# Optimization experiments

Measured on AMD Instinct MI355X. Metric: run time of the kernel, lower is better.

The kernel has to match this reference:

```python
import jax, jax.numpy as jnp
import numpy as np

N_NODES = 50000
N_EDGES = 1_600_000
N_DIMS = 64
INTERACT = ((0,), (1,), (0, 1))  # interact index tuples over [hidden_vi, hidden_vj]


def setup_inputs() -> dict:
    key = jax.random.key(0)
    k1, k2, k3 = jax.random.split(key, 3)
    hidden = jax.random.normal(k1, (1, N_NODES, N_DIMS), dtype=jnp.float32)
    pos_weight = jax.random.uniform(k2, (len(INTERACT), N_DIMS), dtype=jnp.float32)
    neg_weight = jax.random.uniform(k3, (len(INTERACT), N_DIMS), dtype=jnp.float32)
    rng = np.random.default_rng(0)
    vi = np.sort(rng.integers(0, N_NODES, size=N_EDGES)).astype(np.int32)  # sorted by vi
    vj = rng.integers(0, N_NODES, size=N_EDGES).astype(np.int32)
    rel = rng.integers(0, 500, size=N_EDGES).astype(np.int32)
    idx = np.zeros(N_EDGES, dtype=np.int32)  # batch_size == 1
    # (idx, vi, vj, rel, idx_vi, idx_vj, new_idx_e2vi, new_idx_e2vj)
    selected_edges = np.stack([idx, vi, vj, rel, vi, vj, vi, vj], axis=1)
    return {
        "hidden": hidden,
        "pos_weight": pos_weight,
        "neg_weight": neg_weight,
        "selected_edges": jnp.asarray(selected_edges),
    }


def _scorer(inputs, pos_weight, neg_weight):
    # inputs: list of [E, D]; returns per-edge scalar logits [E]
    pos_xs, neg_xs = [], []
    for idxs in INTERACT:
        pos_x = jnp.ones((), jnp.float32)
        neg_x = jnp.ones((), jnp.float32)
        for i in idxs:
            pos_x = pos_x * jnp.maximum(inputs[i], 0)
            neg_x = neg_x * (-jnp.minimum(inputs[i], 0))
        pos_xs.append(pos_x)
        neg_xs.append(neg_x)
    pos_xs = jnp.stack(pos_xs, axis=-2)  # [E, n_prod, D]
    neg_xs = jnp.stack(neg_xs, axis=-2)
    logits = jnp.sum(pos_xs * pos_weight, axis=(-2, -1)) - jnp.sum(neg_xs * neg_weight, axis=(-2, -1))
    return logits  # [E]


def reference(hidden, pos_weight, neg_weight, selected_edges):
    n_nodes = hidden.shape[1]
    vi = selected_edges[:, 1]
    vj = selected_edges[:, 2]
    h = hidden[0]  # [N, D], batch_size == 1

    # node2edge gather
    hidden_vi = h[vi]  # [E, D]
    hidden_vj = h[vj]  # [E, D]

    # per-edge attention logits (Scorer)
    logits = _scorer([hidden_vi, hidden_vj], pos_weight, neg_weight)  # [E]

    # neighbor softmax over outgoing edges of vi (sparse segment softmax)
    seg_max = jax.ops.segment_max(logits, vi, num_segments=n_nodes)
    ex = jnp.exp(logits - seg_max[vi])
    denom = jax.ops.segment_sum(ex, vi, num_segments=n_nodes)
    attn = ex / denom[vi]  # [E]

    # aggregate attended messages at vj and scatter back to node tensor
    msg = attn[:, None] * hidden_vi  # [E, D]
    out = jax.ops.segment_sum(msg, vj, num_segments=n_nodes)  # [N, D]
    return out[None]  # [1, N, D]
```

## Files before the change

kernel.cpp:

```cpp
#include <hip/hip_runtime.h>
#include <math.h>

#define NDIM 64
#define NGRP 8

__device__ __forceinline__ unsigned bf16rne(unsigned u) {
    return (u + 0x7fffu + ((u >> 16) & 1u)) >> 16;
}

__global__ void __launch_bounds__(256)
k_prep_pack(const float* __restrict__ h,
            const float* __restrict__ pw, const float* __restrict__ nw,
            unsigned short* __restrict__ h16, float2* __restrict__ s12,
            const int* __restrict__ edges, unsigned* __restrict__ pvivj,
            int* __restrict__ hist2,
            int n_nodes, int n_edges, int node_blocks) {
    if ((int)blockIdx.x < node_blocks) {
        const int lane = threadIdx.x & 63;
        const int n = blockIdx.x * 4 + (threadIdx.x >> 6);
        if (n >= n_nodes) return;
        const float a = h[(size_t)n * NDIM + lane];
        const float pa = fmaxf(a, 0.f), na = pa - a;
        float t1 = pa * pw[lane]      - na * nw[lane];
        float t2 = pa * pw[64 + lane] - na * nw[64 + lane];
        #pragma unroll
        for (int m = 32; m >= 1; m >>= 1) {
            t1 += __shfl_xor(t1, m, 64);
            t2 += __shfl_xor(t2, m, 64);
        }
        h16[(size_t)n * NDIM + lane] = (unsigned short)bf16rne(__float_as_uint(a));
        if (lane == 0) s12[n] = make_float2(t1, t2);
    } else {
        const int e = ((int)blockIdx.x - node_blocks) * 256 + threadIdx.x;
        if (e >= n_edges) return;
        const int vi = edges[(size_t)e * 8 + 1];
        const int vj = edges[(size_t)e * 8 + 2];
        pvivj[e] = (unsigned)vi | ((unsigned)vj << 16);
        const int g = (e >> 8) & (NGRP - 1);
        atomicAdd(&hist2[g * n_nodes + vj], 1);
    }
}

__global__ void __launch_bounds__(256)
scan_blocks(int* __restrict__ data, int* __restrict__ bsum, int n) {
    __shared__ int sm[256];
    const int t = threadIdx.x;
    const int i = blockIdx.x * 256 + t;
    int v = (i < n) ? data[i] : 0;
    sm[t] = v;
    __syncthreads();
    int x = v;
    #pragma unroll
    for (int off = 1; off < 256; off <<= 1) {
        int add = (t >= off) ? sm[t - off] : 0;
        __syncthreads();
        x += add; sm[t] = x;
        __syncthreads();
    }
    if (i < n) data[i] = x - v;
    if (t == 255) bsum[blockIdx.x] = x;
}

__global__ void __launch_bounds__(256)
scan_top(int* __restrict__ bsum, int nb) {
    __shared__ int sm[256];
    const int t = threadIdx.x;
    const int chunk = (nb + 255) / 256;
    const int beg = t * chunk, end = min(beg + chunk, nb);
    int s = 0;
    for (int i = beg; i < end; ++i) s += bsum[i];
    sm[t] = s;
    __syncthreads();
    int x = s;
    #pragma unroll
    for (int off = 1; off < 256; off <<= 1) {
        int add = (t >= off) ? sm[t - off] : 0;
        __syncthreads();
        x += add; sm[t] = x;
        __syncthreads();
    }
    int run = x - s;
    for (int i = beg; i < end; ++i) { const int v = bsum[i]; bsum[i] = run; run += v; }
}

__global__ void __launch_bounds__(256)
scan_add(int* __restrict__ data, const int* __restrict__ bsum, int n, int total) {
    const int i = blockIdx.x * 256 + threadIdx.x;
    if (i < n) data[i] += bsum[blockIdx.x];
    else if (i == n) data[i] = total;
}

__global__ void __launch_bounds__(256)
k1_fused8(const unsigned* __restrict__ pvivj,
          const unsigned short* __restrict__ h16,
          const float2* __restrict__ s12,
          const float* __restrict__ w2p, const float* __restrict__ w2n,
          float* __restrict__ denom,
          int* __restrict__ offs2,
          unsigned* __restrict__ rec,
          int n_nodes, int n_edges) {
    const int e = blockIdx.x * 256 + threadIdx.x;
    const int lane = threadIdx.x & 63;
    const int ee = min(e, n_edges - 1);
    const unsigned v = pvivj[ee];
    const int vi = (int)(v & 0xffffu), vj = (int)(v >> 16);
    const uint4* hi = (const uint4*)(h16 + (size_t)vi * NDIM);
    const uint4* hj = (const uint4*)(h16 + (size_t)vj * NDIM);
    float cp = 0.f, cn = 0.f;
    #pragma unroll
    for (int q = 0; q < 8; ++q) {
        const uint4 ua = hi[q];
        const uint4 ub = hj[q];
        const unsigned au[4] = {ua.x, ua.y, ua.z, ua.w};
        const unsigned bu[4] = {ub.x, ub.y, ub.z, ub.w};
        #pragma unroll
        for (int k = 0; k < 4; ++k) {
            const int d = q * 8 + k * 2;
            const float a0 = __uint_as_float(au[k] << 16);
            const float a1 = __uint_as_float(au[k] & 0xffff0000u);
            const float b0 = __uint_as_float(bu[k] << 16);
            const float b1 = __uint_as_float(bu[k] & 0xffff0000u);
            const float pa0 = fmaxf(a0, 0.f), na0 = pa0 - a0;
            const float pb0 = fmaxf(b0, 0.f), nb0 = pb0 - b0;
            const float pa1 = fmaxf(a1, 0.f), na1 = pa1 - a1;
            const float pb1 = fmaxf(b1, 0.f), nb1 = pb1 - b1;
            cp = fmaf(pa0 * pb0, w2p[d],     cp);
            cn = fmaf(na0 * nb0, w2n[d],     cn);
            cp = fmaf(pa1 * pb1, w2p[d + 1], cp);
            cn = fmaf(na1 * nb1, w2n[d + 1], cn);
        }
    }
    const float2 si = s12[vi];
    const float2 sj = s12[vj];
    const float exf = (e < n_edges) ? __expf(si.x + sj.y + cp - cn) : 0.f;

    float s = exf;
    #pragma unroll
    for (int o = 1; o < 64; o <<= 1) {
        const float pv = __shfl_up(s, o, 64);
        const int   pi = __shfl_up(vi, o, 64);
        if (lane >= o && pi == vi) s += pv;
    }
    const int nvi = __shfl_down(vi, 1, 64);
    if (lane == 63 || nvi != vi) atomicAdd(&denom[vi], s);

    if (e < n_edges) {
        const int g = blockIdx.x & (NGRP - 1);
        const int pos = atomicAdd(&offs2[g * n_nodes + vj], 1);
        rec[pos] = ((unsigned)vi << 16) | bf16rne(__float_as_uint(exf));
    }
}

__global__ void __launch_bounds__(256)
k_rcp(float* __restrict__ denom, int n) {
    const int i = blockIdx.x * 256 + threadIdx.x;
    if (i < n) {
        const float d = denom[i];
        denom[i] = (d > 0.f) ? 1.f / d : 0.f;
    }
}

__global__ void __launch_bounds__(256)
k3b_gather8(const unsigned* __restrict__ rec, const int* __restrict__ offs2,
            const float* __restrict__ rdenom,
            const unsigned short* __restrict__ h16,
            float* __restrict__ out, int n_nodes) {
    const int lane = threadIdx.x & 63;
    const int n = blockIdx.x * 4 + (threadIdx.x >> 6);
    if (n >= n_nodes) return;
    int begs[NGRP], ends[NGRP];
    #pragma unroll
    for (int g = 0; g < NGRP; ++g) {
        const int i = g * n_nodes + n;
        begs[g] = (i == 0) ? 0 : offs2[i - 1];
        ends[g] = offs2[i];
    }
    float acc = 0.f;
    #pragma unroll
    for (int g = 0; g < NGRP; ++g) {
        int k = begs[g];
        const int end = ends[g];
        for (; k + 2 <= end; k += 2) {
            const unsigned r0 = rec[k], r1 = rec[k + 1];
            const int i0 = (int)(r0 >> 16), i1 = (int)(r1 >> 16);
            const float w0 = __uint_as_float(r0 << 16) * rdenom[i0];
            const float w1 = __uint_as_float(r1 << 16) * rdenom[i1];
            acc = fmaf(w0, __uint_as_float((unsigned)h16[(size_t)i0 * NDIM + lane] << 16), acc);
            acc = fmaf(w1, __uint_as_float((unsigned)h16[(size_t)i1 * NDIM + lane] << 16), acc);
        }
        if (k < end) {
            const unsigned r = rec[k];
            const int i0 = (int)(r >> 16);
            acc = fmaf(__uint_as_float(r << 16) * rdenom[i0],
                       __uint_as_float((unsigned)h16[(size_t)i0 * NDIM + lane] << 16), acc);
        }
    }
    out[(size_t)n * NDIM + lane] = acc;
}

__device__ __forceinline__ float edge_term(float a, float b,
                                           float w0, float w1, float w2,
                                           float w3, float w4, float w5) {
    const float pa = fmaxf(a, 0.f), na = pa - a;
    const float pb = fmaxf(b, 0.f), nb = pb - b;
    return pa * w0 + pb * w1 + (pa * pb) * w2
         - (na * w3 + nb * w4 + (na * nb) * w5);
}

__global__ void __launch_bounds__(256)
k1_full_c(const int* __restrict__ edges, const float* __restrict__ h,
          const float* __restrict__ pw, const float* __restrict__ nw,
          float* __restrict__ ex, int* __restrict__ hist, int n_edges) {
    const int e = blockIdx.x * 256 + threadIdx.x;
    if (e >= n_edges) return;
    const int vi = edges[(size_t)e * 8 + 1];
    const int vj = edges[(size_t)e * 8 + 2];
    const float4* hi = (const float4*)(h + (size_t)vi * NDIM);
    const float4* hj = (const float4*)(h + (size_t)vj * NDIM);
    float c = 0.f;
    #pragma unroll 4
    for (int q = 0; q < 16; ++q) {
        const float4 a = hi[q];
        const float4 b = hj[q];
        const int d = q * 4;
        c += edge_term(a.x, b.x, pw[d],     pw[64 + d],     pw[128 + d],
                                 nw[d],     nw[64 + d],     nw[128 + d]);
        c += edge_term(a.y, b.y, pw[d + 1], pw[64 + d + 1], pw[128 + d + 1],
                                 nw[d + 1], nw[64 + d + 1], nw[128 + d + 1]);
        c += edge_term(a.z, b.z, pw[d + 2], pw[64 + d + 2], pw[128 + d + 2],
                                 nw[d + 2], nw[64 + d + 2], nw[128 + d + 2]);
        c += edge_term(a.w, b.w, pw[d + 3], pw[64 + d + 3], pw[128 + d + 3],
                                 nw[d + 3], nw[64 + d + 3], nw[128 + d + 3]);
    }
    ex[e] = __expf(c);
    atomicAdd(&hist[vj], 1);
}

__global__ void __launch_bounds__(256)
k2_denom_c(const int* __restrict__ edges, const float* __restrict__ ex,
           float* __restrict__ rdenom, int n_edges, int n_nodes) {
    const int n = blockIdx.x * 256 + threadIdx.x;
    if (n >= n_nodes) return;
    int lo = 0, hi = n_edges;
    while (lo < hi) { int mid = (lo + hi) >> 1; if (edges[(size_t)mid * 8 + 1] < n) lo = mid + 1; else hi = mid; }
    const int beg = lo;
    hi = n_edges;
    while (lo < hi) { int mid = (lo + hi) >> 1; if (edges[(size_t)mid * 8 + 1] < n + 1) lo = mid + 1; else hi = mid; }
    const int end = lo;
    float s = 0.f;
    for (int e = beg; e < end; ++e) s += ex[e];
    rdenom[n] = (end > beg) ? 1.f / s : 0.f;
}

__global__ void __launch_bounds__(256)
k3a_scatter_c(const int* __restrict__ edges, const float* __restrict__ ex,
              int* __restrict__ offs, unsigned* __restrict__ rec, int n_edges) {
    const int e = blockIdx.x * 256 + threadIdx.x;
    if (e >= n_edges) return;
    const int vi = edges[(size_t)e * 8 + 1];
    const int vj = edges[(size_t)e * 8 + 2];
    const int pos = atomicAdd(&offs[vj], 1);
    rec[pos] = ((unsigned)vi << 16) | bf16rne(__float_as_uint(ex[e]));
}

__global__ void __launch_bounds__(256)
k3b_gather_c(const unsigned* __restrict__ rec, const int* __restrict__ offs,
             const float* __restrict__ rdenom, const float* __restrict__ h,
             float* __restrict__ out, int n_nodes) {
    const int lane = threadIdx.x & 63;
    const int n = blockIdx.x * 4 + (threadIdx.x >> 6);
    if (n >= n_nodes) return;
    const int beg = (n == 0) ? 0 : offs[n - 1];
    const int end = offs[n];
    float acc = 0.f;
    for (int k = beg; k < end; ++k) {
        const unsigned r = rec[k];
        const int i = (int)(r >> 16);
        acc = fmaf(__uint_as_float(r << 16) * rdenom[i], h[(size_t)i * NDIM + lane], acc);
    }
    out[(size_t)n * NDIM + lane] = acc;
}

extern "C" void kernel_launch(void* const* d_in, const int* in_sizes, int n_in,
                              void* d_out, int out_size, void* d_ws, size_t ws_size,
                              hipStream_t stream) {
    const float* h   = (const float*)d_in[0];
    const float* pw  = (const float*)d_in[1];
    const float* nw  = (const float*)d_in[2];
    const int* edges = (const int*)d_in[3];
    float* out = (float*)d_out;

    const int n_nodes = in_sizes[0] / NDIM;
    const int n_edges = in_sizes[3] / 8;
    const size_t E = (size_t)n_edges, N = (size_t)n_nodes;

    const size_t szPv = E * 4, szRec = E * 4, szH16 = N * NDIM * 2, szS12 = N * 8;
    const size_t szOffs2 = ((size_t)NGRP * N + 1) * 4, szDen = N * 4, szB = 16384;
    const size_t need_A = szPv + szRec + szH16 + szS12 + szOffs2 + szDen + szB;
    const bool tierA = (ws_size >= need_A) && (n_nodes <= 65536);

    const int eb  = (n_edges + 255) / 256;
    const int nbN = (n_nodes + 255) / 256;
    const int nw4 = (n_nodes + 3) / 4;

    if (tierA) {
        char* p = (char*)d_ws;
        unsigned* pvivj = (unsigned*)p;       p += szPv;
        unsigned* rec   = (unsigned*)p;       p += szRec;
        unsigned short* h16 = (unsigned short*)p; p += szH16;
        float2* s12   = (float2*)p;           p += szS12;
        int*    offs2 = (int*)p;              p += szOffs2;
        float*  denom = (float*)p;            p += szDen;
        int*    bsum  = (int*)p;              p += szB;

        hipMemsetAsync(offs2, 0, szOffs2 + szDen, stream);

        k_prep_pack<<<nw4 + eb, 256, 0, stream>>>(h, pw, nw, h16, s12,
                                                  edges, pvivj, offs2,
                                                  n_nodes, n_edges, nw4);
        const int n8 = NGRP * n_nodes;
        const int nb8 = (n8 + 255) / 256;
        scan_blocks<<<nb8, 256, 0, stream>>>(offs2, bsum, n8);
        scan_top<<<1, 256, 0, stream>>>(bsum, nb8);
        scan_add<<<(n8 + 1 + 255) / 256, 256, 0, stream>>>(offs2, bsum, n8, n_edges);

        k1_fused8<<<eb, 256, 0, stream>>>(pvivj, h16, s12, pw + 128, nw + 128,
                                          denom, offs2, rec, n_nodes, n_edges);
        k_rcp<<<nbN, 256, 0, stream>>>(denom, n_nodes);
        k3b_gather8<<<nw4, 256, 0, stream>>>(rec, offs2, denom, h16, out, n_nodes);
    } else {
        char* p = (char*)d_ws;
        float*    ex  = (float*)p;    p += E * 4;
        unsigned* rec = (unsigned*)p; p += E * 4;
        int*   offs   = (int*)p;      p += (N + 1) * 4;
        float* rdenom = (float*)p;    p += N * 4;
        int*   bsum   = (int*)p;      p += 16384;

        hipMemsetAsync(offs, 0, (N + 1) * 4, stream);
        k1_full_c<<<eb, 256, 0, stream>>>(edges, h, pw, nw, ex, offs, n_edges);
        const int nbn = (n_nodes + 255) / 256;
        scan_blocks<<<nbn, 256, 0, stream>>>(offs, bsum, n_nodes);
        scan_top<<<1, 256, 0, stream>>>(bsum, nbn);
        scan_add<<<(n_nodes + 1 + 255) / 256, 256, 0, stream>>>(offs, bsum, n_nodes, n_edges);
        k2_denom_c<<<nbn, 256, 0, stream>>>(edges, ex, rdenom, n_edges, n_nodes);
        k3a_scatter_c<<<eb, 256, 0, stream>>>(edges, ex, offs, rec, n_edges);
        k3b_gather_c<<<nw4, 256, 0, stream>>>(rec, offs, rdenom, h, out, n_nodes);
    }
}
```

Baseline: 273.8 us.

## Bucket CSR by source-node range and gather in per-quarter passes

```diff
diff --git a/kernel.cpp b/kernel.cpp
--- a/kernel.cpp
+++ b/kernel.cpp
@@ -2,7 +2,6 @@
 #include <math.h>
 
 #define NDIM 64
-#define NGRP 8
 
 __device__ __forceinline__ unsigned bf16rne(unsigned u) {
     return (u + 0x7fffu + ((u >> 16) & 1u)) >> 16;
@@ -14,7 +13,7 @@
             unsigned short* __restrict__ h16, float2* __restrict__ s12,
             const int* __restrict__ edges, unsigned* __restrict__ pvivj,
             int* __restrict__ hist2,
-            int n_nodes, int n_edges, int node_blocks) {
+            int n_nodes, int n_edges, int node_blocks, int shift) {
     if ((int)blockIdx.x < node_blocks) {
         const int lane = threadIdx.x & 63;
         const int n = blockIdx.x * 4 + (threadIdx.x >> 6);
@@ -33,11 +32,10 @@
     } else {
         const int e = ((int)blockIdx.x - node_blocks) * 256 + threadIdx.x;
         if (e >= n_edges) return;
-        const int vi = edges[(size_t)e * 8 + 1];
-        const int vj = edges[(size_t)e * 8 + 2];
-        pvivj[e] = (unsigned)vi | ((unsigned)vj << 16);
-        const int g = (e >> 8) & (NGRP - 1);
-        atomicAdd(&hist2[g * n_nodes + vj], 1);
+        const int vi = __builtin_nontemporal_load(edges + (size_t)e * 8 + 1);
+        const int vj = __builtin_nontemporal_load(edges + (size_t)e * 8 + 2);
+        __builtin_nontemporal_store((unsigned)vi | ((unsigned)vj << 16), pvivj + e);
+        atomicAdd(&hist2[(vi >> shift) * n_nodes + vj], 1);
     }
 }
 
@@ -91,18 +89,17 @@
 }
 
 __global__ void __launch_bounds__(256)
-k1_fused8(const unsigned* __restrict__ pvivj,
-          const unsigned short* __restrict__ h16,
-          const float2* __restrict__ s12,
-          const float* __restrict__ w2p, const float* __restrict__ w2n,
-          float* __restrict__ denom,
-          int* __restrict__ offs2,
-          unsigned* __restrict__ rec,
-          int n_nodes, int n_edges) {
+k1_fused(const unsigned* __restrict__ pvivj,
+         const unsigned short* __restrict__ h16,
+         const float2* __restrict__ s12,
+         const float* __restrict__ w2p, const float* __restrict__ w2n,
+         float* __restrict__ denom,
+         int* __restrict__ offs2,
+         unsigned* __restrict__ rec,
+         int n_nodes, int n_edges, int shift) {
     const int e = blockIdx.x * 256 + threadIdx.x;
-    const int lane = threadIdx.x & 63;
-    const int ee = min(e, n_edges - 1);
-    const unsigned v = pvivj[ee];
+    if (e >= n_edges) return;
+    const unsigned v = __builtin_nontemporal_load(pvivj + e);
     const int vi = (int)(v & 0xffffu), vj = (int)(v >> 16);
     const uint4* hi = (const uint4*)(h16 + (size_t)vi * NDIM);
     const uint4* hj = (const uint4*)(h16 + (size_t)vj * NDIM);
@@ -132,23 +129,11 @@
     }
     const float2 si = s12[vi];
     const float2 sj = s12[vj];
-    const float exf = (e < n_edges) ? __expf(si.x + sj.y + cp - cn) : 0.f;
-
-    float s = exf;
-    #pragma unroll
-    for (int o = 1; o < 64; o <<= 1) {
-        const float pv = __shfl_up(s, o, 64);
-        const int   pi = __shfl_up(vi, o, 64);
-        if (lane >= o && pi == vi) s += pv;
-    }
-    const int nvi = __shfl_down(vi, 1, 64);
-    if (lane == 63 || nvi != vi) atomicAdd(&denom[vi], s);
-
-    if (e < n_edges) {
-        const int g = blockIdx.x & (NGRP - 1);
-        const int pos = atomicAdd(&offs2[g * n_nodes + vj], 1);
-        rec[pos] = ((unsigned)vi << 16) | bf16rne(__float_as_uint(exf));
-    }
+    const float exf = __expf(si.x + sj.y + cp - cn);
+    atomicAdd(&denom[vi], exf);
+    const int pos = atomicAdd(&offs2[(vi >> shift) * n_nodes + vj], 1);
+    __builtin_nontemporal_store(((unsigned)vi << 16) | bf16rne(__float_as_uint(exf)),
+                                rec + pos);
 }
 
 __global__ void __launch_bounds__(256)
@@ -160,42 +145,36 @@
     }
 }
 
-__global__ void __launch_bounds__(256)
-k3b_gather8(const unsigned* __restrict__ rec, const int* __restrict__ offs2,
-            const float* __restrict__ rdenom,
-            const unsigned short* __restrict__ h16,
-            float* __restrict__ out, int n_nodes) {
+template <bool ACCUM>
+__global__ void __launch_bounds__(256)
+k3b_pass(const unsigned* __restrict__ rec, const int* __restrict__ offs2,
+         const float* __restrict__ rdenom,
+         const unsigned short* __restrict__ h16,
+         float* __restrict__ out, int n_nodes, int pass_base) {
     const int lane = threadIdx.x & 63;
     const int n = blockIdx.x * 4 + (threadIdx.x >> 6);
     if (n >= n_nodes) return;
-    int begs[NGRP], ends[NGRP];
-    #pragma unroll
-    for (int g = 0; g < NGRP; ++g) {
-        const int i = g * n_nodes + n;
-        begs[g] = (i == 0) ? 0 : offs2[i - 1];
-        ends[g] = offs2[i];
-    }
-    float acc = 0.f;
-    #pragma unroll
-    for (int g = 0; g < NGRP; ++g) {
-        int k = begs[g];
-        const int end = ends[g];
-        for (; k + 2 <= end; k += 2) {
-            const unsigned r0 = rec[k], r1 = rec[k + 1];
-            const int i0 = (int)(r0 >> 16), i1 = (int)(r1 >> 16);
-            const float w0 = __uint_as_float(r0 << 16) * rdenom[i0];
-            const float w1 = __uint_as_float(r1 << 16) * rdenom[i1];
-            acc = fmaf(w0, __uint_as_float((unsigned)h16[(size_t)i0 * NDIM + lane] << 16), acc);
-            acc = fmaf(w1, __uint_as_float((unsigned)h16[(size_t)i1 * NDIM + lane] << 16), acc);
-        }
-        if (k < end) {
-            const unsigned r = rec[k];
-            const int i0 = (int)(r >> 16);
-            acc = fmaf(__uint_as_float(r << 16) * rdenom[i0],
-                       __uint_as_float((unsigned)h16[(size_t)i0 * NDIM + lane] << 16), acc);
-        }
-    }
-    out[(size_t)n * NDIM + lane] = acc;
+    const int i = pass_base + n;
+    const int beg = (i == 0) ? 0 : offs2[i - 1];
+    const int end = offs2[i];
+    float acc = ACCUM ? __builtin_nontemporal_load(out + (size_t)n * NDIM + lane) : 0.f;
+    int k = beg;
+    for (; k + 2 <= end; k += 2) {
+        const unsigned r0 = __builtin_nontemporal_load(rec + k);
+        const unsigned r1 = __builtin_nontemporal_load(rec + k + 1);
+        const int i0 = (int)(r0 >> 16), i1 = (int)(r1 >> 16);
+        const float w0 = __uint_as_float(r0 << 16) * rdenom[i0];
+        const float w1 = __uint_as_float(r1 << 16) * rdenom[i1];
+        acc = fmaf(w0, __uint_as_float((unsigned)h16[(size_t)i0 * NDIM + lane] << 16), acc);
+        acc = fmaf(w1, __uint_as_float((unsigned)h16[(size_t)i1 * NDIM + lane] << 16), acc);
+    }
+    if (k < end) {
+        const unsigned r = __builtin_nontemporal_load(rec + k);
+        const int i0 = (int)(r >> 16);
+        acc = fmaf(__uint_as_float(r << 16) * rdenom[i0],
+                   __uint_as_float((unsigned)h16[(size_t)i0 * NDIM + lane] << 16), acc);
+    }
+    __builtin_nontemporal_store(acc, out + (size_t)n * NDIM + lane);
 }
 
 __device__ __forceinline__ float edge_term(float a, float b,
@@ -294,8 +273,12 @@
     const int n_edges = in_sizes[3] / 8;
     const size_t E = (size_t)n_edges, N = (size_t)n_nodes;
 
+    int shift = 0;
+    while ((1 << shift) < (n_nodes + 3) / 4) ++shift;
+    const int NQ = (n_nodes + (1 << shift) - 1) >> shift;
+
     const size_t szPv = E * 4, szRec = E * 4, szH16 = N * NDIM * 2, szS12 = N * 8;
-    const size_t szOffs2 = ((size_t)NGRP * N + 1) * 4, szDen = N * 4, szB = 16384;
+    const size_t szOffs2 = ((size_t)NQ * N + 1) * 4, szDen = N * 4, szB = 16384;
     const size_t need_A = szPv + szRec + szH16 + szS12 + szOffs2 + szDen + szB;
     const bool tierA = (ws_size >= need_A) && (n_nodes <= 65536);
 
@@ -305,29 +288,33 @@
 
     if (tierA) {
         char* p = (char*)d_ws;
-        unsigned* pvivj = (unsigned*)p;       p += szPv;
-        unsigned* rec   = (unsigned*)p;       p += szRec;
+        unsigned* pvivj = (unsigned*)p;           p += szPv;
+        unsigned* rec   = (unsigned*)p;           p += szRec;
         unsigned short* h16 = (unsigned short*)p; p += szH16;
-        float2* s12   = (float2*)p;           p += szS12;
-        int*    offs2 = (int*)p;              p += szOffs2;
-        float*  denom = (float*)p;            p += szDen;
-        int*    bsum  = (int*)p;              p += szB;
+        float2* s12   = (float2*)p;               p += szS12;
+        int*    offs2 = (int*)p;                  p += szOffs2;
+        float*  denom = (float*)p;                p += szDen;
+        int*    bsum  = (int*)p;                  p += szB;
 
         hipMemsetAsync(offs2, 0, szOffs2 + szDen, stream);
 
         k_prep_pack<<<nw4 + eb, 256, 0, stream>>>(h, pw, nw, h16, s12,
                                                   edges, pvivj, offs2,
-                                                  n_nodes, n_edges, nw4);
-        const int n8 = NGRP * n_nodes;
-        const int nb8 = (n8 + 255) / 256;
-        scan_blocks<<<nb8, 256, 0, stream>>>(offs2, bsum, n8);
-        scan_top<<<1, 256, 0, stream>>>(bsum, nb8);
-        scan_add<<<(n8 + 1 + 255) / 256, 256, 0, stream>>>(offs2, bsum, n8, n_edges);
-
-        k1_fused8<<<eb, 256, 0, stream>>>(pvivj, h16, s12, pw + 128, nw + 128,
-                                          denom, offs2, rec, n_nodes, n_edges);
+                                                  n_nodes, n_edges, nw4, shift);
+        const int nQ = NQ * n_nodes;
+        const int nbQ = (nQ + 255) / 256;
+        scan_blocks<<<nbQ, 256, 0, stream>>>(offs2, bsum, nQ);
+        scan_top<<<1, 256, 0, stream>>>(bsum, nbQ);
+        scan_add<<<(nQ + 1 + 255) / 256, 256, 0, stream>>>(offs2, bsum, nQ, n_edges);
+
+        k1_fused<<<eb, 256, 0, stream>>>(pvivj, h16, s12, pw + 128, nw + 128,
+                                         denom, offs2, rec, n_nodes, n_edges, shift);
         k_rcp<<<nbN, 256, 0, stream>>>(denom, n_nodes);
-        k3b_gather8<<<nw4, 256, 0, stream>>>(rec, offs2, denom, h16, out, n_nodes);
+
+        k3b_pass<false><<<nw4, 256, 0, stream>>>(rec, offs2, denom, h16, out, n_nodes, 0);
+        for (int q = 1; q < NQ; ++q)
+            k3b_pass<true><<<nw4, 256, 0, stream>>>(rec, offs2, denom, h16, out,
+                                                    n_nodes, q * n_nodes);
     } else {
         char* p = (char*)d_ws;
         float*    ex  = (float*)p;    p += E * 4;
@@ -338,11 +325,10 @@
 
         hipMemsetAsync(offs, 0, (N + 1) * 4, stream);
         k1_full_c<<<eb, 256, 0, stream>>>(edges, h, pw, nw, ex, offs, n_edges);
-        const int nbn = (n_nodes + 255) / 256;
-        scan_blocks<<<nbn, 256, 0, stream>>>(offs, bsum, n_nodes);
-        scan_top<<<1, 256, 0, stream>>>(bsum, nbn);
+        scan_blocks<<<nbN, 256, 0, stream>>>(offs, bsum, n_nodes);
+        scan_top<<<1, 256, 0, stream>>>(bsum, nbN);
         scan_add<<<(n_nodes + 1 + 255) / 256, 256, 0, stream>>>(offs, bsum, n_nodes, n_edges);
-        k2_denom_c<<<nbn, 256, 0, stream>>>(edges, ex, rdenom, n_edges, n_nodes);
+        k2_denom_c<<<nbN, 256, 0, stream>>>(edges, ex, rdenom, n_edges, n_nodes);
         k3a_scatter_c<<<eb, 256, 0, stream>>>(edges, ex, offs, rec, n_edges);
         k3b_gather_c<<<nw4, 256, 0, stream>>>(rec, offs, rdenom, h, out, n_nodes);
     }
```

Measured after the change: 497.7 us. 1.82x slower.
